# Kernel tuning notes

Hardware: AMD Instinct MI355X
Metric: run time of the kernel (lower is better)

## Reference

```python
import jax, jax.numpy as jnp
import numpy as np

S, B, H, V, L = 128, 32, 512, 10000, 2

def setup_inputs() -> dict:
    key = jax.random.key(0)
    ks = jax.random.split(key, 8)
    u = float(np.sqrt(1.0 / H))
    return {
        "tokens": jax.random.randint(ks[0], (S, B), 0, V, dtype=jnp.int64),
        "h0": jnp.zeros((L, B, H), dtype=jnp.float32),
        "emb": jax.random.normal(ks[1], (V, H), dtype=jnp.float32) * 0.1,
        "Wx": jax.random.uniform(ks[2], (L, 3, H, H), minval=-u, maxval=u, dtype=jnp.float32),
        "bx": jax.random.uniform(ks[3], (L, 3, H), minval=-u, maxval=u, dtype=jnp.float32),
        "U": jax.random.uniform(ks[4], (L, 3, H, H), minval=-u, maxval=u, dtype=jnp.float32),
        "Wy": jax.random.uniform(ks[5], (V, H), minval=-u, maxval=u, dtype=jnp.float32),
        "by": jax.random.uniform(ks[6], (V,), minval=-u, maxval=u, dtype=jnp.float32),
    }

def _gru_cell(x, h, Wx, bx, U):
    # x,h: [B,H]; Wx,U: [3,H,H]; bx: [3,H]
    ax = jnp.einsum('bi,gio->bgo', x, Wx) + bx  # [B,3,H]
    r = jax.nn.sigmoid(ax[:, 0] + h @ U[0])
    z = jax.nn.sigmoid(ax[:, 1] + h @ U[1])
    h_hat = jnp.tanh(ax[:, 2] + (r * h) @ U[2])
    return (1.0 - z) * h + z * h_hat

def reference(tokens, h0, emb, Wx, bx, U, Wy, by):
    embs = emb[tokens]  # [S,B,H]

    def step(h_stack, x_t):
        new_h = []
        inp = x_t
        for l in range(L):
            h_l = _gru_cell(inp, h_stack[l], Wx[l], bx[l], U[l])
            new_h.append(h_l)
            inp = h_l
        return jnp.stack(new_h), inp  # carry, top-layer output

    h_final, tops = jax.lax.scan(step, h0, embs)  # tops: [S,B,H]
    logits = jnp.einsum('sbh,vh->sbv', tops, Wy) + by  # [S,B,V]
    return logits, h_final
```

## Files before the change

kernel.cpp:

```cpp
#include <hip/hip_runtime.h>
#include <cmath>

#define S_LEN 128
#define BATCH 32
#define HID   512
#define VOCAB 10000
#define MROWS (S_LEN * BATCH)
#define HH    (HID * HID)

#define NBLK  64
#define NTHR  512

typedef float f32x4 __attribute__((ext_vector_type(4)));

template<bool GATHER_A, bool B_KN>
__global__ __launch_bounds__(256) void gemm_kernel(
    const float* __restrict__ A, const int* __restrict__ tok,
    const float* __restrict__ Bmat, const float* __restrict__ bias,
    float* __restrict__ C, int M, int N, int K)
{
    __shared__ float As[32][68];
    __shared__ float Bs[32][68];
    __shared__ int   toks[64];

    const int tid = threadIdx.x;
    const int m0  = blockIdx.y * 64;
    const int n0  = blockIdx.x * 64;

    if (GATHER_A && tid < 64) toks[tid] = tok[m0 + tid];
    __syncthreads();

    const int tx = tid & 15;
    const int ty = tid >> 4;
    const int lr = tid >> 3;
    const int lc = (tid & 7) * 4;

    float acc[4][4] = {};

    for (int k0 = 0; k0 < K; k0 += 32) {
        #pragma unroll
        for (int rep = 0; rep < 2; rep++) {
            int r = lr + rep * 32;
            const float* arow;
            if (GATHER_A) arow = A + (size_t)toks[r] * K;
            else          arow = A + (size_t)(m0 + r) * K;
            float4 v = *(const float4*)(arow + k0 + lc);
            As[lc + 0][r] = v.x; As[lc + 1][r] = v.y;
            As[lc + 2][r] = v.z; As[lc + 3][r] = v.w;
        }
        if (B_KN) {
            int g    = n0 >> 9;
            int col0 = n0 & 511;
            const float* bbase = Bmat + (size_t)g * K * 512 + col0;
            int bc = (tid & 15) * 4;
            int bk = tid >> 4;
            #pragma unroll
            for (int rep = 0; rep < 2; rep++) {
                int kk = bk + rep * 16;
                float4 v = *(const float4*)(bbase + (size_t)(k0 + kk) * 512 + bc);
                *(float4*)&Bs[kk][bc] = v;
            }
        } else {
            #pragma unroll
            for (int rep = 0; rep < 2; rep++) {
                int r = lr + rep * 32;
                int n = n0 + r;
                float4 v = make_float4(0.f, 0.f, 0.f, 0.f);
                if (n < N) v = *(const float4*)(Bmat + (size_t)n * K + k0 + lc);
                Bs[lc + 0][r] = v.x; Bs[lc + 1][r] = v.y;
                Bs[lc + 2][r] = v.z; Bs[lc + 3][r] = v.w;
            }
        }
        __syncthreads();
        #pragma unroll
        for (int k = 0; k < 32; k++) {
            float4 a4 = *(const float4*)&As[k][ty * 4];
            float4 b4 = *(const float4*)&Bs[k][tx * 4];
            float av[4] = {a4.x, a4.y, a4.z, a4.w};
            float bv[4] = {b4.x, b4.y, b4.z, b4.w};
            #pragma unroll
            for (int i = 0; i < 4; i++)
                #pragma unroll
                for (int j = 0; j < 4; j++)
                    acc[i][j] = fmaf(av[i], bv[j], acc[i][j]);
        }
        __syncthreads();
    }
    #pragma unroll
    for (int i = 0; i < 4; i++) {
        int m = m0 + ty * 4 + i;
        #pragma unroll
        for (int j = 0; j < 4; j++) {
            int n = n0 + tx * 4 + j;
            if (n < N) C[(size_t)m * N + n] = acc[i][j] + bias[n];
        }
    }
}

__device__ __forceinline__ f32x4 ldg_coh_x4(const float* p) {
    f32x4 r;
    asm volatile("global_load_dwordx4 %0, %1, off sc1"
                 : "=v"(r) : "v"(p) : "memory");
    return r;
}
__device__ __forceinline__ void stg_coh(float* p, float v) {
    asm volatile("global_store_dword %0, %1, off sc1"
                 :: "v"(p), "v"(v) : "memory");
}

__device__ __forceinline__ void flag_bar(unsigned* flags, int bid, unsigned target)
{
    asm volatile("s_waitcnt vmcnt(0)" ::: "memory");
    __syncthreads();
    if (threadIdx.x == 0)
        __hip_atomic_store(&flags[bid], target, __ATOMIC_RELEASE, __HIP_MEMORY_SCOPE_AGENT);
    if (threadIdx.x < NBLK) {
        while (__hip_atomic_load(&flags[threadIdx.x], __ATOMIC_RELAXED,
                                 __HIP_MEMORY_SCOPE_AGENT) < target)
            __builtin_amdgcn_s_sleep(1);
    }
    __syncthreads();
}

__global__ __launch_bounds__(NTHR) void scan_coop_kernel(
    const float* __restrict__ ax, const float* __restrict__ Ul,
    const float* __restrict__ h0g, float* __restrict__ hseq,
    float* __restrict__ hfin, float* __restrict__ vT,
    float* __restrict__ hxT, unsigned* __restrict__ flags)
{
    __shared__ float Wrz[512 * 16];
    __shared__ float Whh[512 * 8];
    __shared__ float xbuf[512 * 32];
    __shared__ float part[16 * 512];
    __shared__ float partR[2048];
    __shared__ float zbuf[8 * 33];
    __shared__ float hsave[8 * 33];

    const int tid = threadIdx.x;
    const int bid = blockIdx.x;
    const int ch0 = bid << 3;

    const int bt  = tid & 7;
    const int ct  = (tid >> 3) & 3;
    const int ks  = tid >> 5;
    const int ct2 = (tid >> 3) & 1;
    const int ks2 = tid >> 4;
    const int rb  = tid & 31;
    const int rc  = tid >> 5;

    for (int idx = tid; idx < 512 * 16; idx += NTHR) {
        int c = idx & 15, k = idx >> 4;
        Wrz[k * 16 + c] = Ul[(size_t)(c >> 3) * HH + (size_t)k * HID + ch0 + (c & 7)];
    }
    for (int idx = tid; idx < 512 * 8; idx += NTHR) {
        int c = idx & 7, k = idx >> 3;
        int cs = (((c >> 2) ^ ((k >> 4) & 1)) << 2) | (c & 3);
        Whh[k * 8 + cs] = Ul[(size_t)2 * HH + (size_t)k * HID + ch0 + c];
    }

    if (tid < 256) {
        int c = tid >> 5, b = tid & 31;
        stg_coh(hxT + (ch0 + c) * 32 + b, h0g[b * HID + ch0 + c]);
    }
    unsigned bc = 1;
    flag_bar(flags, bid, bc); bc++;

    for (int t = 0; t < S_LEN; t++) {
        const size_t axrow = (size_t)((t << 5) + rb) * 1536;
        const float ax1 = ax[axrow + (rc < 8 ? ch0 + rc : 512 + ch0 + (rc - 8))];
        const float ax2 = (tid < 256) ? ax[axrow + 1024 + ch0 + (tid >> 5)] : 0.f;

        {
            f32x4 ld[8];
            #pragma unroll
            for (int i = 0; i < 8; i++)
                ld[i] = ldg_coh_x4(hxT + (size_t)(tid + i * NTHR) * 4);
            asm volatile("s_waitcnt vmcnt(0)" ::: "memory");
            #pragma unroll
            for (int i = 0; i < 8; i++)
                *(f32x4*)&xbuf[(tid + i * NTHR) * 4] = ld[i];
        }
        __syncthreads();

        {
            f32x4 a0 = {0.f,0.f,0.f,0.f}, a1 = a0, a2 = a0, a3 = a0;
            const int kb = ks << 5;
            #pragma unroll
            for (int kk = 0; kk < 32; kk++) {
                int k = kb + kk;
                f32x4 wv = *(const f32x4*)&Wrz[(k << 4) + (ct << 2)];
                f32x4 xv = *(const f32x4*)&xbuf[(k << 5) + (bt << 2)];
                a0 += wv.x * xv;
                a1 += wv.y * xv;
                a2 += wv.z * xv;
                a3 += wv.w * xv;
            }
            const int c0 = ct << 2;
            *(f32x4*)&part[(ks << 9) + ((c0    ) << 5) + (bt << 2)] = a0;
            *(f32x4*)&part[(ks << 9) + ((c0 + 1) << 5) + (bt << 2)] = a1;
            *(f32x4*)&part[(ks << 9) + ((c0 + 2) << 5) + (bt << 2)] = a2;
            *(f32x4*)&part[(ks << 9) + ((c0 + 3) << 5) + (bt << 2)] = a3;
        }
        __syncthreads();

        {
            const int out4 = tid & 127;
            const int qh   = tid >> 7;
            f32x4 s = {0.f,0.f,0.f,0.f};
            #pragma unroll
            for (int j = 0; j < 4; j++)
                s += *(const f32x4*)&part[((qh << 2) + j) * 512 + (out4 << 2)];
            *(f32x4*)&partR[(qh << 9) + (out4 << 2)] = s;
        }
        __syncthreads();

        {
            float s = partR[(rc << 5) + rb] + partR[512 + (rc << 5) + rb]
                    + partR[1024 + (rc << 5) + rb] + partR[1536 + (rc << 5) + rb];
            float sig = 1.f / (1.f + __expf(-(ax1 + s)));
            if (rc < 8) {
                float hk = xbuf[((ch0 + rc) << 5) + rb];
                stg_coh(vT + (ch0 + rc) * 32 + rb, sig * hk);
            } else {
                zbuf[(rc - 8) * 33 + rb]  = sig;
                hsave[(rc - 8) * 33 + rb] = xbuf[((ch0 + rc - 8) << 5) + rb];
            }
        }
        flag_bar(flags, bid, bc); bc++;

        {
            f32x4 ld[8];
            #pragma unroll
            for (int i = 0; i < 8; i++)
                ld[i] = ldg_coh_x4(vT + (size_t)(tid + i * NTHR) * 4);
            asm volatile("s_waitcnt vmcnt(0)" ::: "memory");
            #pragma unroll
            for (int i = 0; i < 8; i++)
                *(f32x4*)&xbuf[(tid + i * NTHR) * 4] = ld[i];
        }
        __syncthreads();

        {
            f32x4 a0 = {0.f,0.f,0.f,0.f}, a1 = a0, a2 = a0, a3 = a0;
            const int kb = ks2 << 4;
            #pragma unroll
            for (int kk = 0; kk < 16; kk++) {
                int k = kb + kk;
                int wch = ((ct2 ^ ((k >> 4) & 1)) << 2);
                f32x4 wv = *(const f32x4*)&Whh[(k << 3) + wch];
                f32x4 xv = *(const f32x4*)&xbuf[(k << 5) + (bt << 2)];
                a0 += wv.x * xv;
                a1 += wv.y * xv;
                a2 += wv.z * xv;
                a3 += wv.w * xv;
            }
            const int c0 = ct2 << 2;
            *(f32x4*)&part[(ks2 << 8) + ((c0    ) << 5) + (bt << 2)] = a0;
            *(f32x4*)&part[(ks2 << 8) + ((c0 + 1) << 5) + (bt << 2)] = a1;
            *(f32x4*)&part[(ks2 << 8) + ((c0 + 2) << 5) + (bt << 2)] = a2;
            *(f32x4*)&part[(ks2 << 8) + ((c0 + 3) << 5) + (bt << 2)] = a3;
        }
        __syncthreads();

        {
            const int out4 = tid & 63;
            const int qh   = tid >> 6;
            f32x4 s = {0.f,0.f,0.f,0.f};
            #pragma unroll
            for (int j = 0; j < 4; j++)
                s += *(const f32x4*)&part[((qh << 2) + j) * 256 + (out4 << 2)];
            *(f32x4*)&partR[(qh << 8) + (out4 << 2)] = s;
        }
        __syncthreads();

        if (tid < 256) {
            const int c = tid >> 5, b = tid & 31;
            float s = 0.f;
            #pragma unroll
            for (int qh = 0; qh < 8; qh++) s += partR[(qh << 8) + (c << 5) + b];
            float pre = ax2 + s;
            float e2  = __expf(2.f * pre);
            float hh  = 1.f - 2.f / (e2 + 1.f);
            float z   = zbuf[c * 33 + b];
            float h   = hsave[c * 33 + b];
            float hn  = (1.f - z) * h + z * hh;
            stg_coh(hxT + (ch0 + c) * 32 + b, hn);
            part[c * 33 + b] = hn;
            if (t == S_LEN - 1) hfin[b * HID + ch0 + c] = hn;
        }
        __syncthreads();
        if (tid < 256) {
            const int c = tid & 7, b = tid >> 3;
            hseq[(size_t)((t << 5) + b) * HID + ch0 + c] = part[c * 33 + b];
        }
        flag_bar(flags, bid, bc); bc++;
    }
}

extern "C" void kernel_launch(void* const* d_in, const int* in_sizes, int n_in,
                              void* d_out, int out_size, void* d_ws, size_t ws_size,
                              hipStream_t stream)
{
    const int*   tokens = (const int*)  d_in[0];
    const float* h0     = (const float*)d_in[1];
    const float* emb    = (const float*)d_in[2];
    const float* Wx     = (const float*)d_in[3];
    const float* bx     = (const float*)d_in[4];
    const float* U      = (const float*)d_in[5];
    const float* Wy     = (const float*)d_in[6];
    const float* by     = (const float*)d_in[7];
    float*       out    = (float*)d_out;

    float* ws    = (float*)d_ws;
    float* axbuf = ws;
    float* hseq  = axbuf + (size_t)MROWS * 1536;

    const size_t logits_sz = (size_t)MROWS * VOCAB;
    float* hfin0 = out + logits_sz;
    float* hfin1 = out + logits_sz + BATCH * HID;

    float*    vT    = out;
    float*    hxT   = out + 16384;
    unsigned* flags = (unsigned*)(out + 32768);
    hipMemsetAsync(flags, 0, 2 * NBLK * sizeof(unsigned), stream);

    gemm_kernel<true, true><<<dim3(1536 / 64, MROWS / 64), 256, 0, stream>>>(
        emb, tokens, Wx, bx, axbuf, MROWS, 1536, HID);

    scan_coop_kernel<<<NBLK, NTHR, 0, stream>>>(
        axbuf, U, h0, hseq, hfin0, vT, hxT, flags);

    gemm_kernel<false, true><<<dim3(1536 / 64, MROWS / 64), 256, 0, stream>>>(
        hseq, nullptr, Wx + 3 * HH, bx + 1536, axbuf, MROWS, 1536, HID);

    scan_coop_kernel<<<NBLK, NTHR, 0, stream>>>(
        axbuf, U + 3 * HH, h0 + BATCH * HID, hseq, hfin1, vT, hxT, flags + NBLK);

    gemm_kernel<false, false><<<dim3((VOCAB + 63) / 64, MROWS / 64), 256, 0, stream>>>(
        hseq, nullptr, Wy, by, out, MROWS, VOCAB, HID);
}
```

Measured before the change: 4.202 ms.

## Split grid barriers to overlap z-gate work, transpose ax, add 128-tile logits GEMM

The cooperative scan now splits each grid barrier into arrive and wait halves. The z-gate matvec runs between arrive and wait after r is published, and the hseq store plus the prefetch of the next step's ax values sit inside the second barrier window. The input-projection GEMMs write ax transposed, so each scan thread reads its gate preactivations with coalesced accesses. The final vocabulary GEMM moves to a new 128x128-tile kernel with 8x8 per-thread accumulators, raising register use in exchange for more data reuse.

```diff
diff --git a/kernel.cpp b/kernel.cpp
--- a/kernel.cpp
+++ b/kernel.cpp
@@ -13,7 +13,7 @@
 
 typedef float f32x4 __attribute__((ext_vector_type(4)));
 
-template<bool GATHER_A, bool B_KN>
+template<bool GATHER_A, bool B_KN, bool C_T>
 __global__ __launch_bounds__(256) void gemm_kernel(
     const float* __restrict__ A, const int* __restrict__ tok,
     const float* __restrict__ Bmat, const float* __restrict__ bias,
@@ -86,13 +86,94 @@
         }
         __syncthreads();
     }
-    #pragma unroll
-    for (int i = 0; i < 4; i++) {
-        int m = m0 + ty * 4 + i;
+    if (C_T) {
         #pragma unroll
         for (int j = 0; j < 4; j++) {
             int n = n0 + tx * 4 + j;
-            if (n < N) C[(size_t)m * N + n] = acc[i][j] + bias[n];
+            float bn = bias[n];
+            float4 v = make_float4(acc[0][j] + bn, acc[1][j] + bn,
+                                   acc[2][j] + bn, acc[3][j] + bn);
+            *(float4*)&C[(size_t)n * M + m0 + ty * 4] = v;
+        }
+    } else {
+        #pragma unroll
+        for (int i = 0; i < 4; i++) {
+            int m = m0 + ty * 4 + i;
+            #pragma unroll
+            for (int j = 0; j < 4; j++) {
+                int n = n0 + tx * 4 + j;
+                if (n < N) C[(size_t)m * N + n] = acc[i][j] + bias[n];
+            }
+        }
+    }
+}
+
+__global__ __launch_bounds__(256) void gemm128_kernel(
+    const float* __restrict__ A, const float* __restrict__ B,
+    const float* __restrict__ bias, float* __restrict__ C,
+    int M, int N, int K)
+{
+    __shared__ float As[16][132];
+    __shared__ float Bs[16][132];
+
+    const int tid = threadIdx.x;
+    const int m0  = blockIdx.y * 128;
+    const int n0  = blockIdx.x * 128;
+    const int tx  = tid & 15;
+    const int ty  = tid >> 4;
+    const int lr  = tid >> 2;
+    const int lc  = (tid & 3) * 4;
+
+    float acc[8][8] = {};
+
+    for (int k0 = 0; k0 < K; k0 += 16) {
+        #pragma unroll
+        for (int rep = 0; rep < 2; rep++) {
+            int r = lr + rep * 64;
+            float4 va = *(const float4*)(A + (size_t)(m0 + r) * K + k0 + lc);
+            As[lc + 0][r] = va.x; As[lc + 1][r] = va.y;
+            As[lc + 2][r] = va.z; As[lc + 3][r] = va.w;
+            int n = n0 + r;
+            float4 vb = make_float4(0.f, 0.f, 0.f, 0.f);
+            if (n < N) vb = *(const float4*)(B + (size_t)n * K + k0 + lc);
+            Bs[lc + 0][r] = vb.x; Bs[lc + 1][r] = vb.y;
+            Bs[lc + 2][r] = vb.z; Bs[lc + 3][r] = vb.w;
+        }
+        __syncthreads();
+        #pragma unroll
+        for (int k = 0; k < 16; k++) {
+            f32x4 a0 = *(const f32x4*)&As[k][ty * 8];
+            f32x4 a1 = *(const f32x4*)&As[k][ty * 8 + 4];
+            f32x4 b0 = *(const f32x4*)&Bs[k][tx * 8];
+            f32x4 b1 = *(const f32x4*)&Bs[k][tx * 8 + 4];
+            float av[8] = {a0.x,a0.y,a0.z,a0.w,a1.x,a1.y,a1.z,a1.w};
+            float bv[8] = {b0.x,b0.y,b0.z,b0.w,b1.x,b1.y,b1.z,b1.w};
+            #pragma unroll
+            for (int i = 0; i < 8; i++)
+                #pragma unroll
+                for (int j = 0; j < 8; j++)
+                    acc[i][j] = fmaf(av[i], bv[j], acc[i][j]);
+        }
+        __syncthreads();
+    }
+    const bool full = (n0 + 128 <= N);
+    #pragma unroll
+    for (int i = 0; i < 8; i++) {
+        int m = m0 + ty * 8 + i;
+        if (full) {
+            int n = n0 + tx * 8;
+            float4 v0 = make_float4(acc[i][0]+bias[n+0], acc[i][1]+bias[n+1],
+                                    acc[i][2]+bias[n+2], acc[i][3]+bias[n+3]);
+            float4 v1 = make_float4(acc[i][4]+bias[n+4], acc[i][5]+bias[n+5],
+                                    acc[i][6]+bias[n+6], acc[i][7]+bias[n+7]);
+            *(float4*)&C[(size_t)m * N + n]     = v0;
+            *(float4*)&C[(size_t)m * N + n + 4] = v1;
+        } else {
+            #pragma unroll
+            for (int j = 0; j < 8; j++) {
+                int n = n0 + tx * 8 + j;
+                if (n < N) C[(size_t)m * N + n] = acc[i][j] + bias[n];
+            }
         }
     }
 }
@@ -108,12 +189,15 @@
                  :: "v"(p), "v"(v) : "memory");
 }
 
-__device__ __forceinline__ void flag_bar(unsigned* flags, int bid, unsigned target)
+__device__ __forceinline__ void bar_arrive(unsigned* flags, int bid, unsigned target)
 {
     asm volatile("s_waitcnt vmcnt(0)" ::: "memory");
     __syncthreads();
     if (threadIdx.x == 0)
         __hip_atomic_store(&flags[bid], target, __ATOMIC_RELEASE, __HIP_MEMORY_SCOPE_AGENT);
+}
+__device__ __forceinline__ void bar_wait(unsigned* flags, unsigned target)
+{
     if (threadIdx.x < NBLK) {
         while (__hip_atomic_load(&flags[threadIdx.x], __ATOMIC_RELAXED,
                                  __HIP_MEMORY_SCOPE_AGENT) < target)
@@ -123,53 +207,54 @@
 }
 
 __global__ __launch_bounds__(NTHR) void scan_coop_kernel(
-    const float* __restrict__ ax, const float* __restrict__ Ul,
+    const float* __restrict__ axT, const float* __restrict__ Ul,
     const float* __restrict__ h0g, float* __restrict__ hseq,
     float* __restrict__ hfin, float* __restrict__ vT,
     float* __restrict__ hxT, unsigned* __restrict__ flags)
 {
-    __shared__ float Wrz[512 * 16];
-    __shared__ float Whh[512 * 8];
+    __shared__ float Wr[512 * 8];
+    __shared__ float Wz[512 * 8];
+    __shared__ float Wh[512 * 8];
     __shared__ float xbuf[512 * 32];
-    __shared__ float part[16 * 512];
-    __shared__ float partR[2048];
+    __shared__ float part[32 * 256];
+    __shared__ float partR[8 * 256];
     __shared__ float zbuf[8 * 33];
     __shared__ float hsave[8 * 33];
+    __shared__ float hnb[8 * 33];
 
     const int tid = threadIdx.x;
     const int bid = blockIdx.x;
     const int ch0 = bid << 3;
 
     const int bt  = tid & 7;
-    const int ct  = (tid >> 3) & 3;
-    const int ks  = tid >> 5;
-    const int ct2 = (tid >> 3) & 1;
-    const int ks2 = tid >> 4;
+    const int ct1 = (tid >> 3) & 1;
+    const int ks  = tid >> 4;
+    const int wsel = ((ct1 ^ ks) & 1) << 2;
+    const int rc  = tid >> 5;
     const int rb  = tid & 31;
-    const int rc  = tid >> 5;
-
-    for (int idx = tid; idx < 512 * 16; idx += NTHR) {
-        int c = idx & 15, k = idx >> 4;
-        Wrz[k * 16 + c] = Ul[(size_t)(c >> 3) * HH + (size_t)k * HID + ch0 + (c & 7)];
-    }
+
     for (int idx = tid; idx < 512 * 8; idx += NTHR) {
         int c = idx & 7, k = idx >> 3;
-        int cs = (((c >> 2) ^ ((k >> 4) & 1)) << 2) | (c & 3);
-        Whh[k * 8 + cs] = Ul[(size_t)2 * HH + (size_t)k * HID + ch0 + c];
-    }
-
+        int p = (k << 3) + ((((c >> 2) ^ (k >> 4)) & 1) << 2) + (c & 3);
+        Wr[p] = Ul[                (size_t)k * HID + ch0 + c];
+        Wz[p] = Ul[(size_t)1 * HH + (size_t)k * HID + ch0 + c];
+        Wh[p] = Ul[(size_t)2 * HH + (size_t)k * HID + ch0 + c];
+    }
+
+    if (tid < 256)
+        stg_coh(hxT + (ch0 + rc) * 32 + rb, h0g[rb * HID + ch0 + rc]);
+    unsigned bc = 1;
+    bar_arrive(flags, bid, bc);
+
+    float axr = 0.f, axz = 0.f, axh = 0.f;
     if (tid < 256) {
-        int c = tid >> 5, b = tid & 31;
-        stg_coh(hxT + (ch0 + c) * 32 + b, h0g[b * HID + ch0 + c]);
-    }
-    unsigned bc = 1;
-    flag_bar(flags, bid, bc); bc++;
+        axr = axT[(size_t)(       ch0 + rc) * MROWS + rb];
+        axz = axT[(size_t)( 512 + ch0 + rc) * MROWS + rb];
+        axh = axT[(size_t)(1024 + ch0 + rc) * MROWS + rb];
+    }
+    bar_wait(flags, bc); bc++;
 
     for (int t = 0; t < S_LEN; t++) {
-        const size_t axrow = (size_t)((t << 5) + rb) * 1536;
-        const float ax1 = ax[axrow + (rc < 8 ? ch0 + rc : 512 + ch0 + (rc - 8))];
-        const float ax2 = (tid < 256) ? ax[axrow + 1024 + ch0 + (tid >> 5)] : 0.f;
-
         {
             f32x4 ld[8];
             #pragma unroll
@@ -184,49 +269,76 @@
 
         {
             f32x4 a0 = {0.f,0.f,0.f,0.f}, a1 = a0, a2 = a0, a3 = a0;
-            const int kb = ks << 5;
-            #pragma unroll
-            for (int kk = 0; kk < 32; kk++) {
+            const int kb = ks << 4;
+            #pragma unroll
+            for (int kk = 0; kk < 16; kk++) {
                 int k = kb + kk;
-                f32x4 wv = *(const f32x4*)&Wrz[(k << 4) + (ct << 2)];
+                f32x4 wv = *(const f32x4*)&Wr[(k << 3) + wsel];
                 f32x4 xv = *(const f32x4*)&xbuf[(k << 5) + (bt << 2)];
-                a0 += wv.x * xv;
-                a1 += wv.y * xv;
-                a2 += wv.z * xv;
-                a3 += wv.w * xv;
-            }
-            const int c0 = ct << 2;
-            *(f32x4*)&part[(ks << 9) + ((c0    ) << 5) + (bt << 2)] = a0;
-            *(f32x4*)&part[(ks << 9) + ((c0 + 1) << 5) + (bt << 2)] = a1;
-            *(f32x4*)&part[(ks << 9) + ((c0 + 2) << 5) + (bt << 2)] = a2;
-            *(f32x4*)&part[(ks << 9) + ((c0 + 3) << 5) + (bt << 2)] = a3;
-        }
-        __syncthreads();
-
-        {
-            const int out4 = tid & 127;
-            const int qh   = tid >> 7;
+                a0 += wv.x * xv; a1 += wv.y * xv;
+                a2 += wv.z * xv; a3 += wv.w * xv;
+            }
+            const int c0 = ct1 << 2;
+            *(f32x4*)&part[(ks << 8) + ((c0    ) << 5) + (bt << 2)] = a0;
+            *(f32x4*)&part[(ks << 8) + ((c0 + 1) << 5) + (bt << 2)] = a1;
+            *(f32x4*)&part[(ks << 8) + ((c0 + 2) << 5) + (bt << 2)] = a2;
+            *(f32x4*)&part[(ks << 8) + ((c0 + 3) << 5) + (bt << 2)] = a3;
+        }
+        __syncthreads();
+        {
+            const int out4 = tid & 63, qh = tid >> 6;
             f32x4 s = {0.f,0.f,0.f,0.f};
             #pragma unroll
             for (int j = 0; j < 4; j++)
-                s += *(const f32x4*)&part[((qh << 2) + j) * 512 + (out4 << 2)];
-            *(f32x4*)&partR[(qh << 9) + (out4 << 2)] = s;
-        }
-        __syncthreads();
-
-        {
-            float s = partR[(rc << 5) + rb] + partR[512 + (rc << 5) + rb]
-                    + partR[1024 + (rc << 5) + rb] + partR[1536 + (rc << 5) + rb];
-            float sig = 1.f / (1.f + __expf(-(ax1 + s)));
-            if (rc < 8) {
-                float hk = xbuf[((ch0 + rc) << 5) + rb];
-                stg_coh(vT + (ch0 + rc) * 32 + rb, sig * hk);
-            } else {
-                zbuf[(rc - 8) * 33 + rb]  = sig;
-                hsave[(rc - 8) * 33 + rb] = xbuf[((ch0 + rc - 8) << 5) + rb];
-            }
-        }
-        flag_bar(flags, bid, bc); bc++;
+                s += *(const f32x4*)&part[(((qh << 2) + j) << 8) + (out4 << 2)];
+            *(f32x4*)&partR[(qh << 8) + (out4 << 2)] = s;
+        }
+        __syncthreads();
+        if (tid < 256) {
+            float s = 0.f;
+            #pragma unroll
+            for (int qh = 0; qh < 8; qh++) s += partR[(qh << 8) + (rc << 5) + rb];
+            float sig = 1.f / (1.f + __expf(-(axr + s)));
+            float hk  = xbuf[((ch0 + rc) << 5) + rb];
+            stg_coh(vT + (ch0 + rc) * 32 + rb, sig * hk);
+        }
+        bar_arrive(flags, bid, bc);
+
+        {
+            f32x4 a0 = {0.f,0.f,0.f,0.f}, a1 = a0, a2 = a0, a3 = a0;
+            const int kb = ks << 4;
+            #pragma unroll
+            for (int kk = 0; kk < 16; kk++) {
+                int k = kb + kk;
+                f32x4 wv = *(const f32x4*)&Wz[(k << 3) + wsel];
+                f32x4 xv = *(const f32x4*)&xbuf[(k << 5) + (bt << 2)];
+                a0 += wv.x * xv; a1 += wv.y * xv;
+                a2 += wv.z * xv; a3 += wv.w * xv;
+            }
+            const int c0 = ct1 << 2;
+            *(f32x4*)&part[(ks << 8) + ((c0    ) << 5) + (bt << 2)] = a0;
+            *(f32x4*)&part[(ks << 8) + ((c0 + 1) << 5) + (bt << 2)] = a1;
+            *(f32x4*)&part[(ks << 8) + ((c0 + 2) << 5) + (bt << 2)] = a2;
+            *(f32x4*)&part[(ks << 8) + ((c0 + 3) << 5) + (bt << 2)] = a3;
+        }
+        __syncthreads();
+        {
+            const int out4 = tid & 63, qh = tid >> 6;
+            f32x4 s = {0.f,0.f,0.f,0.f};
+            #pragma unroll
+            for (int j = 0; j < 4; j++)
+                s += *(const f32x4*)&part[(((qh << 2) + j) << 8) + (out4 << 2)];
+            *(f32x4*)&partR[(qh << 8) + (out4 << 2)] = s;
+        }
+        __syncthreads();
+        if (tid < 256) {
+            float s = 0.f;
+            #pragma unroll
+            for (int qh = 0; qh < 8; qh++) s += partR[(qh << 8) + (rc << 5) + rb];
+            zbuf[rc * 33 + rb]  = 1.f / (1.f + __expf(-(axz + s)));
+            hsave[rc * 33 + rb] = xbuf[((ch0 + rc) << 5) + rb];
+        }
+        bar_wait(flags, bc); bc++;
 
         {
             f32x4 ld[8];
@@ -242,58 +354,58 @@
 
         {
             f32x4 a0 = {0.f,0.f,0.f,0.f}, a1 = a0, a2 = a0, a3 = a0;
-            const int kb = ks2 << 4;
+            const int kb = ks << 4;
             #pragma unroll
             for (int kk = 0; kk < 16; kk++) {
                 int k = kb + kk;
-                int wch = ((ct2 ^ ((k >> 4) & 1)) << 2);
-                f32x4 wv = *(const f32x4*)&Whh[(k << 3) + wch];
+                f32x4 wv = *(const f32x4*)&Wh[(k << 3) + wsel];
                 f32x4 xv = *(const f32x4*)&xbuf[(k << 5) + (bt << 2)];
-                a0 += wv.x * xv;
-                a1 += wv.y * xv;
-                a2 += wv.z * xv;
-                a3 += wv.w * xv;
-            }
-            const int c0 = ct2 << 2;
-            *(f32x4*)&part[(ks2 << 8) + ((c0    ) << 5) + (bt << 2)] = a0;
-            *(f32x4*)&part[(ks2 << 8) + ((c0 + 1) << 5) + (bt << 2)] = a1;
-            *(f32x4*)&part[(ks2 << 8) + ((c0 + 2) << 5) + (bt << 2)] = a2;
-            *(f32x4*)&part[(ks2 << 8) + ((c0 + 3) << 5) + (bt << 2)] = a3;
-        }
-        __syncthreads();
-
-        {
-            const int out4 = tid & 63;
-            const int qh   = tid >> 6;
+                a0 += wv.x * xv; a1 += wv.y * xv;
+                a2 += wv.z * xv; a3 += wv.w * xv;
+            }
+            const int c0 = ct1 << 2;
+            *(f32x4*)&part[(ks << 8) + ((c0    ) << 5) + (bt << 2)] = a0;
+            *(f32x4*)&part[(ks << 8) + ((c0 + 1) << 5) + (bt << 2)] = a1;
+            *(f32x4*)&part[(ks << 8) + ((c0 + 2) << 5) + (bt << 2)] = a2;
+            *(f32x4*)&part[(ks << 8) + ((c0 + 3) << 5) + (bt << 2)] = a3;
+        }
+        __syncthreads();
+        {
+            const int out4 = tid & 63, qh = tid >> 6;
             f32x4 s = {0.f,0.f,0.f,0.f};
             #pragma unroll
             for (int j = 0; j < 4; j++)
-                s += *(const f32x4*)&part[((qh << 2) + j) * 256 + (out4 << 2)];
+                s += *(const f32x4*)&part[(((qh << 2) + j) << 8) + (out4 << 2)];
             *(f32x4*)&partR[(qh << 8) + (out4 << 2)] = s;
         }
         __syncthreads();
-
         if (tid < 256) {
-            const int c = tid >> 5, b = tid & 31;
             float s = 0.f;
             #pragma unroll
-            for (int qh = 0; qh < 8; qh++) s += partR[(qh << 8) + (c << 5) + b];
-            float pre = ax2 + s;
+            for (int qh = 0; qh < 8; qh++) s += partR[(qh << 8) + (rc << 5) + rb];
+            float pre = axh + s;
             float e2  = __expf(2.f * pre);
             float hh  = 1.f - 2.f / (e2 + 1.f);
-            float z   = zbuf[c * 33 + b];
-            float h   = hsave[c * 33 + b];
+            float z   = zbuf[rc * 33 + rb];
+            float h   = hsave[rc * 33 + rb];
             float hn  = (1.f - z) * h + z * hh;
-            stg_coh(hxT + (ch0 + c) * 32 + b, hn);
-            part[c * 33 + b] = hn;
-            if (t == S_LEN - 1) hfin[b * HID + ch0 + c] = hn;
-        }
-        __syncthreads();
+            stg_coh(hxT + (ch0 + rc) * 32 + rb, hn);
+            hnb[rc * 33 + rb] = hn;
+            if (t == S_LEN - 1) hfin[rb * HID + ch0 + rc] = hn;
+        }
+        bar_arrive(flags, bid, bc);
+
         if (tid < 256) {
-            const int c = tid & 7, b = tid >> 3;
-            hseq[(size_t)((t << 5) + b) * HID + ch0 + c] = part[c * 33 + b];
-        }
-        flag_bar(flags, bid, bc); bc++;
+            const int c2 = tid & 7, b2 = tid >> 3;
+            hseq[(size_t)((t << 5) + b2) * HID + ch0 + c2] = hnb[c2 * 33 + b2];
+            if (t + 1 < S_LEN) {
+                const size_t o = (size_t)((t + 1) << 5) + rb;
+                axr = axT[(size_t)(       ch0 + rc) * MROWS + o];
+                axz = axT[(size_t)( 512 + ch0 + rc) * MROWS + o];
+                axh = axT[(size_t)(1024 + ch0 + rc) * MROWS + o];
+            }
+        }
+        bar_wait(flags, bc); bc++;
     }
 }
 
@@ -312,8 +424,8 @@
     float*       out    = (float*)d_out;
 
     float* ws    = (float*)d_ws;
-    float* axbuf = ws;
-    float* hseq  = axbuf + (size_t)MROWS * 1536;
+    float* axT   = ws;
+    float* hseq  = axT + (size_t)1536 * MROWS;
 
     const size_t logits_sz = (size_t)MROWS * VOCAB;
     float* hfin0 = out + logits_sz;
@@ -324,18 +436,18 @@
     unsigned* flags = (unsigned*)(out + 32768);
     hipMemsetAsync(flags, 0, 2 * NBLK * sizeof(unsigned), stream);
 
-    gemm_kernel<true, true><<<dim3(1536 / 64, MROWS / 64), 256, 0, stream>>>(
-        emb, tokens, Wx, bx, axbuf, MROWS, 1536, HID);
+    gemm_kernel<true, true, true><<<dim3(1536 / 64, MROWS / 64), 256, 0, stream>>>(
+        emb, tokens, Wx, bx, axT, MROWS, 1536, HID);
 
     scan_coop_kernel<<<NBLK, NTHR, 0, stream>>>(
-        axbuf, U, h0, hseq, hfin0, vT, hxT, flags);
-
-    gemm_kernel<false, true><<<dim3(1536 / 64, MROWS / 64), 256, 0, stream>>>(
-        hseq, nullptr, Wx + 3 * HH, bx + 1536, axbuf, MROWS, 1536, HID);
+        axT, U, h0, hseq, hfin0, vT, hxT, flags);
+
+    gemm_kernel<false, true, true><<<dim3(1536 / 64, MROWS / 64), 256, 0, stream>>>(
+        hseq, nullptr, Wx + 3 * HH, bx + 1536, axT, MROWS, 1536, HID);
 
     scan_coop_kernel<<<NBLK, NTHR, 0, stream>>>(
-        axbuf, U + 3 * HH, h0 + BATCH * HID, hseq, hfin1, vT, hxT, flags + NBLK);
-
-    gemm_kernel<false, false><<<dim3((VOCAB + 63) / 64, MROWS / 64), 256, 0, stream>>>(
-        hseq, nullptr, Wy, by, out, MROWS, VOCAB, HID);
-}
+        axT, U + 3 * HH, h0 + BATCH * HID, hseq, hfin1, vT, hxT, flags + NBLK);
+
+    gemm128_kernel<<<dim3((VOCAB + 127) / 128, MROWS / 128), 256, 0, stream>>>(
+        hseq, Wy, by, out, MROWS, VOCAB, HID);
+}
```

Result: faster. 3.453 ms (-17.8%).
